# Performance work log

Measured on AMD Instinct MI355X. Metric: run time of the kernel, lower is better.

Reference implementation:

```python
import jax, jax.numpy as jnp
import numpy as np

B, T, C = 2, 2048, 1024
LAT = 256
N_HEAD = 16
HEAD_DIM = C // N_HEAD
SCALE = 1.0 / np.sqrt(HEAD_DIM).astype(np.float32)


def setup_inputs() -> dict:
    key = jax.random.key(0)
    ks = jax.random.split(key, 9)
    s_in = 0.02  # small init so softmax is well-conditioned
    return {
        "x": jax.random.normal(ks[0], (B, T, C), dtype=jnp.float32),
        "wq_lat": jax.random.normal(ks[1], (C, LAT), dtype=jnp.float32) * s_in,
        "wk_lat": jax.random.normal(ks[2], (C, LAT), dtype=jnp.float32) * s_in,
        "wv_lat": jax.random.normal(ks[3], (C, LAT), dtype=jnp.float32) * s_in,
        "wq_heads": jax.random.normal(ks[4], (LAT, C), dtype=jnp.float32) * s_in,
        "wk_heads": jax.random.normal(ks[5], (LAT, C), dtype=jnp.float32) * s_in,
        "wv_heads": jax.random.normal(ks[6], (LAT, C), dtype=jnp.float32) * s_in,
        "w_proj": jax.random.normal(ks[7], (C, C), dtype=jnp.float32) * s_in,
        "b_proj": jnp.zeros((C,), dtype=jnp.float32),
    }


def reference(x, wq_lat, wk_lat, wv_lat, wq_heads, wk_heads, wv_heads, w_proj, b_proj):
    Bx, Tx, Cx = x.shape
    # low-rank latent projections then up-projection to per-head q/k/v
    q = (x @ wq_lat) @ wq_heads  # [B,T,C]
    k = (x @ wk_lat) @ wk_heads
    v = (x @ wv_lat) @ wv_heads
    q = q.reshape(Bx, Tx, N_HEAD, HEAD_DIM).transpose(0, 2, 1, 3)  # [B,H,T,D]
    k = k.reshape(Bx, Tx, N_HEAD, HEAD_DIM).transpose(0, 2, 1, 3)
    v = v.reshape(Bx, Tx, N_HEAD, HEAD_DIM).transpose(0, 2, 1, 3)
    att = jnp.einsum("bhqd,bhkd->bhqk", q, k) * SCALE  # [B,H,T,T]
    causal = jnp.tril(jnp.ones((Tx, Tx), dtype=bool))
    att = jnp.where(causal[None, None], att, -jnp.inf)
    att = jax.nn.softmax(att, axis=-1)
    y = jnp.einsum("bhqk,bhkd->bhqd", att, v)  # [B,H,T,D]
    y = y.transpose(0, 2, 1, 3).reshape(Bx, Tx, Cx)
    return y @ w_proj + b_proj
```

## Files before the change

kernel.cpp:

```cpp
#include <hip/hip_runtime.h>

#define SCALE 0.125f
#define SL 0.18033688011112042f

typedef __bf16 bf16x8 __attribute__((ext_vector_type(8)));
typedef short short4v __attribute__((ext_vector_type(4)));
typedef unsigned short u16x4 __attribute__((ext_vector_type(4)));
typedef float f32x4 __attribute__((ext_vector_type(4)));
typedef unsigned int uint2v __attribute__((ext_vector_type(2)));

__device__ __forceinline__ unsigned short f2b(float f) {
  unsigned u = __float_as_uint(f);
  u += 0x7fffu + ((u >> 16) & 1u);
  return (unsigned short)(u >> 16);
}
__device__ __forceinline__ float ex2(float x) {
  float r;
  asm("v_exp_f32 %0, %1" : "=v"(r) : "v"(x));
  return r;
}

#define GLB(p) ((__attribute__((address_space(1))) void*)(void*)(p))
#define LDSP(p) ((__attribute__((address_space(3))) void*)(p))

__global__ __launch_bounds__(256) void prep(
    const float* __restrict__ x, const float* __restrict__ wq_lat,
    const float* __restrict__ wk_lat, const float* __restrict__ wv_lat,
    const float* __restrict__ wq_h, const float* __restrict__ wk_h,
    const float* __restrict__ wv_h, const float* __restrict__ w_proj,
    unsigned short* __restrict__ x_bf, unsigned short* __restrict__ wlatT,
    unsigned short* __restrict__ whT, unsigned short* __restrict__ wpT) {
  __shared__ float tile[32][33];
  const int blk = blockIdx.x, tid = threadIdx.x;
  if (blk < 1024) {
    int i = blk * 256 + tid;
#pragma unroll
    for (int j = 0; j < 4; j++) {
      float4 v = ((const float4*)x)[i + j * 262144];
      u16x4 p;
      p.x = f2b(v.x); p.y = f2b(v.y); p.z = f2b(v.z); p.w = f2b(v.w);
      ((u16x4*)x_bf)[i + j * 262144] = p;
    }
  } else if (blk < 1792) {
    int idx = blk - 1024;
    int z = idx >> 8, rem = idx & 255;
    const float* wsrc = z == 0 ? wq_lat : (z == 1 ? wk_lat : wv_lat);
    unsigned short* o = wlatT + z * 262144;
    int c0 = (rem & 7) * 32, r0 = (rem >> 3) * 32;
    int tx = tid & 31, ty = tid >> 5;
#pragma unroll
    for (int i = 0; i < 32; i += 8) tile[ty + i][tx] = wsrc[(r0 + ty + i) * 256 + c0 + tx];
    __syncthreads();
#pragma unroll
    for (int i = 0; i < 32; i += 8) o[(c0 + ty + i) * 1024 + r0 + tx] = f2b(tile[tx][ty + i]);
  } else if (blk < 2560) {
    int idx = blk - 1792;
    int z = idx >> 8, rem = idx & 255;
    const float* wsrc = z == 0 ? wq_h : (z == 1 ? wk_h : wv_h);
    unsigned short* o = whT + z * 262144;
    int c0 = (rem & 31) * 32, r0 = (rem >> 5) * 32;
    int tx = tid & 31, ty = tid >> 5;
#pragma unroll
    for (int i = 0; i < 32; i += 8) tile[ty + i][tx] = wsrc[(r0 + ty + i) * 1024 + c0 + tx];
    __syncthreads();
#pragma unroll
    for (int i = 0; i < 32; i += 8) o[(c0 + ty + i) * 256 + r0 + tx] = f2b(tile[tx][ty + i]);
  } else {
    int idx = blk - 2560;
    int c0 = (idx & 31) * 32, r0 = (idx >> 5) * 32;
    int tx = tid & 31, ty = tid >> 5;
#pragma unroll
    for (int i = 0; i < 32; i += 8) tile[ty + i][tx] = w_proj[(r0 + ty + i) * 1024 + c0 + tx];
    __syncthreads();
#pragma unroll
    for (int i = 0; i < 32; i += 8) wpT[(c0 + ty + i) * 1024 + r0 + tx] = f2b(tile[tx][ty + i]);
  }
}

template <int MODE>
__global__ __launch_bounds__(256) void gemm_bt(
    const unsigned short* __restrict__ A0, const unsigned short* __restrict__ A1,
    const unsigned short* __restrict__ A2,
    const unsigned short* __restrict__ B0, const unsigned short* __restrict__ B1,
    const unsigned short* __restrict__ B2,
    void* __restrict__ C0, void* __restrict__ C1, void* __restrict__ C2,
    const float* __restrict__ bias, int M, int N, int K) {
  const int z = blockIdx.z;
  const unsigned short* A = z == 0 ? A0 : (z == 1 ? A1 : A2);
  const unsigned short* BT = z == 0 ? B0 : (z == 1 ? B1 : B2);
  void* C = z == 0 ? C0 : (z == 1 ? C1 : C2);

  __shared__ unsigned short lA[128 * 32];
  __shared__ unsigned short lB[128 * 32];

  const int t = threadIdx.x;
  const int n0 = blockIdx.x * 128;
  const int m0 = blockIdx.y * 128;
  const int lane = t & 63;
  const int wid = t >> 6;
  const int wr = wid >> 1, wc = wid & 1;
  const int lo = lane & 15, g = lane >> 4;

  f32x4 acc[4][4];
#pragma unroll
  for (int i = 0; i < 4; i++)
#pragma unroll
    for (int j = 0; j < 4; j++) acc[i][j] = (f32x4){0.f, 0.f, 0.f, 0.f};

  const unsigned short* ga = A + (size_t)(m0 + (t >> 2)) * K + (t & 3) * 8;
  const unsigned short* gb = BT + (size_t)(n0 + (t >> 2)) * K + (t & 3) * 8;
  const size_t rowK64 = (size_t)64 * K;

  for (int k0 = 0; k0 < K; k0 += 32) {
    __syncthreads();
    __builtin_amdgcn_global_load_lds(GLB(ga + k0), LDSP((char*)lA + t * 16), 16, 0, 0);
    __builtin_amdgcn_global_load_lds(GLB(ga + rowK64 + k0), LDSP((char*)lA + 4096 + t * 16), 16, 0, 0);
    __builtin_amdgcn_global_load_lds(GLB(gb + k0), LDSP((char*)lB + t * 16), 16, 0, 0);
    __builtin_amdgcn_global_load_lds(GLB(gb + rowK64 + k0), LDSP((char*)lB + 4096 + t * 16), 16, 0, 0);
    __syncthreads();

    bf16x8 af[4], bfr[4];
#pragma unroll
    for (int i = 0; i < 4; i++) {
      af[i] = *(const bf16x8*)&lA[(wr * 64 + i * 16 + lo) * 32 + g * 8];
      bfr[i] = *(const bf16x8*)&lB[(wc * 64 + i * 16 + lo) * 32 + g * 8];
    }
#pragma unroll
    for (int i = 0; i < 4; i++)
#pragma unroll
      for (int j = 0; j < 4; j++)
        acc[i][j] = __builtin_amdgcn_mfma_f32_16x16x32_bf16(af[i], bfr[j], acc[i][j], 0, 0, 0);
  }

  if constexpr (MODE == 2) {
    float* Cf = (float*)C;
#pragma unroll
    for (int i = 0; i < 4; i++) {
      int row0 = m0 + wr * 64 + i * 16 + g * 4;
#pragma unroll
      for (int j = 0; j < 4; j++) {
        int col = n0 + wc * 64 + j * 16 + lo;
        float bv = bias[col];
#pragma unroll
        for (int r = 0; r < 4; r++) Cf[(size_t)(row0 + r) * N + col] = acc[i][j][r] + bv;
      }
    }
  } else {
    unsigned short* Cb = (unsigned short*)C;
#pragma unroll
    for (int i = 0; i < 4; i++) {
      int row0 = m0 + wr * 64 + i * 16 + g * 4;
#pragma unroll
      for (int j = 0; j < 4; j++) {
        int col = n0 + wc * 64 + j * 16 + lo;
#pragma unroll
        for (int r = 0; r < 4; r++) Cb[(size_t)(row0 + r) * N + col] = f2b(acc[i][j][r]);
      }
    }
  }
}

__global__ __launch_bounds__(512) void gemm_up8(const unsigned short* __restrict__ A,
                                                const unsigned short* __restrict__ BT,
                                                unsigned short* __restrict__ Qo,
                                                unsigned short* __restrict__ Ko,
                                                unsigned short* __restrict__ Vo) {
  __shared__ char smem[131072];

  const int t = threadIdx.x;
  const int lane = t & 63;
  const int wid = t >> 6;
  const int wr = wid >> 2, wc = wid & 3;
  const int lo = lane & 15, g = lane >> 4;
  const int lin = blockIdx.x;
  const int xcd = lin & 7;
  const int slot = lin >> 3;
  const int by = (xcd << 1) | (slot >= 12 ? 1 : 0);
  const int bx = slot >= 12 ? slot - 12 : slot;
  const int m0 = by * 256;
  const int z = bx >> 2;
  const int ncb = (bx & 3) * 256;
  const unsigned short* Az = A + (size_t)z * 1048576;
  const unsigned short* Bz = BT + (size_t)z * 262144;

  const int slog8 = (((t & 3) ^ ((t >> 2) & 3) ^ (((t >> 4) & 1) << 1)) << 3);
  const unsigned short *aS00, *aS01, *aS10, *aS11, *bS00, *bS01, *bS10, *bS11;
  {
    const int r = t >> 2;
    aS00 = Az + (size_t)(m0 + r) * 256 + slog8;
    aS01 = Az + (size_t)(m0 + r + 128) * 256 + slog8;
    aS10 = aS00 + 32;
    aS11 = aS01 + 32;
    bS00 = Bz + (size_t)(ncb + r) * 256 + slog8;
    bS01 = Bz + (size_t)(ncb + r + 128) * 256 + slog8;
    bS10 = bS00 + 32;
    bS11 = bS01 + 32;
  }
  char* dA0 = smem + t * 16;
  char* dA1 = smem + 16384 + t * 16;
  char* dB0 = smem + 32768 + t * 16;
  char* dB1 = smem + 49152 + t * 16;

  const int slotA = ((g ^ (lo & 3) ^ (((lo >> 2) & 1) << 1)) << 4);
  const char* aR = smem + (wr * 128 + lo) * 64 + slotA;
  const char* bR = smem + 32768 + (wc * 64 + lo) * 64 + slotA;

  f32x4 acc[8][4];
#pragma unroll
  for (int i = 0; i < 8; i++)
#pragma unroll
    for (int j = 0; j < 4; j++) acc[i][j] = (f32x4){0.f, 0.f, 0.f, 0.f};

#define STG(p0, p1, dst, D)                                                              \
  __builtin_amdgcn_global_load_lds(GLB(p0), LDSP(dst + (D)*65536), 16, 0, 0);            \
  __builtin_amdgcn_global_load_lds(GLB(p1), LDSP(dst + (D)*65536 + 8192), 16, 0, 0);     \
  p0 += 64; p1 += 64;

#define MF16(FRB, af, bf)                                                                \
  __builtin_amdgcn_s_setprio(1);                                                         \
  _Pragma("unroll") for (int i = 0; i < 4; i++)                                          \
  _Pragma("unroll") for (int j = 0; j < 4; j++)                                          \
      acc[(FRB) + i][j] = __builtin_amdgcn_mfma_f32_16x16x32_bf16(af[i], bf[j],          \
                                                                  acc[(FRB) + i][j], 0, 0, 0); \
  __builtin_amdgcn_s_setprio(0);

#define TILE(D, S)                                                                       \
  {                                                                                      \
    bf16x8 af[4], bf[4];                                                                 \
    _Pragma("unroll") for (int j = 0; j < 4; j++)                                        \
        bf[j] = *(const bf16x8*)(bR + (D)*65536 + j * 1024);                             \
    _Pragma("unroll") for (int i = 0; i < 4; i++)                                        \
        af[i] = *(const bf16x8*)(aR + (D)*65536 + i * 1024);                             \
    if (S) { STG(aS00, aS01, dA0, (D) ^ 1); }                                            \
    __builtin_amdgcn_s_barrier();                                                        \
    MF16(0, af, bf);                                                                     \
    __builtin_amdgcn_s_barrier();                                                        \
    _Pragma("unroll") for (int i = 0; i < 4; i++)                                        \
        af[i] = *(const bf16x8*)(aR + (D)*65536 + (4 + i) * 1024);                       \
    if (S) { STG(bS00, bS01, dB0, (D) ^ 1); }                                            \
    __builtin_amdgcn_s_barrier();                                                        \
    MF16(4, af, bf);                                                                     \
    if (S) { asm volatile("s_waitcnt vmcnt(4)" ::: "memory"); }                          \
    else   { asm volatile("s_waitcnt vmcnt(0)" ::: "memory"); }                          \
    __builtin_amdgcn_s_barrier();                                                        \
    _Pragma("unroll") for (int j = 0; j < 4; j++)                                        \
        bf[j] = *(const bf16x8*)(bR + (D)*65536 + 16384 + j * 1024);                     \
    _Pragma("unroll") for (int i = 0; i < 4; i++)                                        \
        af[i] = *(const bf16x8*)(aR + (D)*65536 + 16384 + i * 1024);                     \
    if (S) { STG(aS10, aS11, dA1, (D) ^ 1); }                                            \
    __builtin_amdgcn_s_barrier();                                                        \
    MF16(0, af, bf);                                                                     \
    __builtin_amdgcn_s_barrier();                                                        \
    _Pragma("unroll") for (int i = 0; i < 4; i++)                                        \
        af[i] = *(const bf16x8*)(aR + (D)*65536 + 16384 + (4 + i) * 1024);               \
    if (S) { STG(bS10, bS11, dB1, (D) ^ 1); }                                            \
    __builtin_amdgcn_s_barrier();                                                        \
    MF16(4, af, bf);                                                                     \
    if (S) { asm volatile("s_waitcnt vmcnt(4)" ::: "memory"); }                          \
    __builtin_amdgcn_s_barrier();                                                        \
  }

  { STG(aS00, aS01, dA0, 0); }
  { STG(bS00, bS01, dB0, 0); }
  { STG(aS10, aS11, dA1, 0); }
  { STG(bS10, bS11, dB1, 0); }
  asm volatile("s_waitcnt vmcnt(0)" ::: "memory");
  __builtin_amdgcn_s_barrier();

  TILE(0, 1);
  TILE(1, 1);
  TILE(0, 1);
  TILE(1, 0);

#undef TILE
#undef MF16
#undef STG

  if (z < 2) {
    unsigned short* Cb = z == 0 ? Qo : Ko;
    const float scl = z == 0 ? SL : 1.0f;
#pragma unroll
    for (int fr = 0; fr < 8; fr++) {
      int row0 = m0 + wr * 128 + fr * 16 + g * 4;
#pragma unroll
      for (int fc = 0; fc < 4; fc++) {
        int col = ncb + wc * 64 + fc * 16 + lo;
#pragma unroll
        for (int r = 0; r < 4; r++) Cb[(size_t)(row0 + r) * 1024 + col] = f2b(acc[fr][fc][r] * scl);
      }
    }
  } else {
#pragma unroll
    for (int fr = 0; fr < 8; fr++) {
      int row0 = m0 + wr * 128 + fr * 16 + g * 4;
      int bb = row0 >> 11, tloc = row0 & 2047;
#pragma unroll
      for (int fc = 0; fc < 4; fc++) {
        int col = ncb + wc * 64 + fc * 16 + lo;
        u16x4 pk;
#pragma unroll
        for (int r = 0; r < 4; r++) pk[r] = f2b(acc[fr][fc][r]);
        *(u16x4*)&Vo[((size_t)(bb * 1024) + col) * 2048 + tloc] = pk;
      }
    }
  }
}

__global__ __launch_bounds__(256) void attn_fwd(const unsigned short* __restrict__ Q,
                                                const unsigned short* __restrict__ K,
                                                const unsigned short* __restrict__ VT,
                                                unsigned short* __restrict__ Y) {
  __shared__ char smem[32768];

  const int tid = threadIdx.x;
  const int w = tid >> 6;
  const int lane = tid & 63;
  const int lo = lane & 15, g = lane >> 4;
  const int lo7 = lo & 7;
  const int bid = blockIdx.x;
  const int bh = bid & 31;
  const int code = bid >> 5;
  const int qq = code >> 3, kk = code & 7;
  const int chunk = qq == 0 ? 31 - kk : (qq == 1 ? 16 + kk : (qq == 2 ? 15 - kk : kk));
  const int b = bh >> 4, h = bh & 15;
  const int q0 = chunk * 64 + w * 16;

  const unsigned short* Qb = Q + (size_t)(b * 2048) * 1024 + h * 64;
  const unsigned short* Kb = K + (size_t)(b * 2048) * 1024 + h * 64;
  const unsigned short* Vb = VT + (size_t)((b * 16 + h) * 64) * 2048;

  bf16x8 qf0 = *(const bf16x8*)(Qb + (size_t)(q0 + lo) * 1024 + g * 8);
  bf16x8 qf1 = *(const bf16x8*)(Qb + (size_t)(q0 + lo) * 1024 + 32 + g * 8);

  const f32x4 z4 = (f32x4){0.f, 0.f, 0.f, 0.f};
  f32x4 acc[4];
#pragma unroll
  for (int dt = 0; dt < 4; dt++) acc[dt] = z4;
  float lrun = 0.f;
  const int nt = chunk + 1;

  const int koff = lo * 128 + ((g ^ lo7) << 4);
  char* kb0 = smem + koff;
  char* kb1 = smem + (koff ^ 64);
  const int voff = lo * 128 + ((g ^ ((lo7 & 1) << 1)) << 3) + ((lo7 >> 1) << 5);
  char* vq0 = smem + 16384 + voff;
  char* vq1 = smem + 16384 + (voff ^ 32);
  char* vq2 = smem + 16384 + (voff ^ 64);
  char* vq3 = smem + 16384 + (voff ^ 96);

  const int r0s = tid >> 3, c0s = (tid & 7) ^ (r0s & 7);
  const unsigned short* sk0 = Kb + (size_t)r0s * 1024 + c0s * 8;
  const unsigned short* sk1 = sk0 + (size_t)32 * 1024;
  const unsigned short* sv0 = Vb + (size_t)r0s * 2048 + c0s * 8;
  const unsigned short* sv1 = sv0 + (size_t)32 * 2048;
  char* dk0 = smem + tid * 16;
  char* dk1 = smem + 4096 + tid * 16;
  char* dv0 = smem + 16384 + tid * 16;
  char* dv1 = smem + 20480 + tid * 16;

#define STAGE(BUF)                                                                        \
  __builtin_amdgcn_global_load_lds(GLB(sk0), LDSP(dk0 + (BUF)*8192), 16, 0, 0);           \
  __builtin_amdgcn_global_load_lds(GLB(sk1), LDSP(dk1 + (BUF)*8192), 16, 0, 0);           \
  __builtin_amdgcn_global_load_lds(GLB(sv0), LDSP(dv0 + (BUF)*8192), 16, 0, 0);           \
  __builtin_amdgcn_global_load_lds(GLB(sv1), LDSP(dv1 + (BUF)*8192), 16, 0, 0);           \
  sk0 += 65536; sk1 += 65536; sv0 += 64; sv1 += 64;

#define COMPUTE(k0v, BUF, MASKED)                                                         \
  {                                                                                       \
    bf16x8 kfA[4], kfB[4];                                                                \
    _Pragma("unroll") for (int kvf = 0; kvf < 4; kvf++) {                                 \
      kfA[kvf] = *(const bf16x8*)(kb0 + (BUF)*8192 + kvf * 2048);                         \
      kfB[kvf] = *(const bf16x8*)(kb1 + (BUF)*8192 + kvf * 2048);                         \
    }                                                                                     \
    short4v vf[4][4];                                                                     \
    _Pragma("unroll") for (int kvf = 0; kvf < 4; kvf++) {                                 \
      const char* vp = kvf == 0 ? vq0 : (kvf == 1 ? vq1 : (kvf == 2 ? vq2 : vq3));        \
      _Pragma("unroll") for (int dt = 0; dt < 4; dt++)                                    \
          vf[dt][kvf] = *(const short4v*)(vp + (BUF)*8192 + dt * 2048);                   \
    }                                                                                     \
    f32x4 st[4];                                                                          \
    __builtin_amdgcn_s_setprio(1);                                                        \
    _Pragma("unroll") for (int kvf = 0; kvf < 4; kvf++) {                                 \
      st[kvf] = __builtin_amdgcn_mfma_f32_16x16x32_bf16(kfA[kvf], qf0, z4, 0, 0, 0);      \
      st[kvf] = __builtin_amdgcn_mfma_f32_16x16x32_bf16(kfB[kvf], qf1, st[kvf], 0, 0, 0); \
    }                                                                                     \
    __builtin_amdgcn_s_setprio(0);                                                        \
    if (MASKED) {                                                                         \
      const int qg = q0 + lo;                                                             \
      _Pragma("unroll") for (int kvf = 0; kvf < 4; kvf++)                                 \
      _Pragma("unroll") for (int r = 0; r < 4; r++) {                                     \
        int tk = (k0v) + kvf * 16 + g * 4 + r;                                            \
        if (tk > qg) st[kvf][r] = -3.0e38f;                                               \
      }                                                                                   \
    }                                                                                     \
    __builtin_amdgcn_s_setprio(1);                                                        \
    _Pragma("unroll") for (int kvf = 0; kvf < 4; kvf++) {                                 \
      float p0 = ex2(st[kvf][0]);                                                         \
      float p1 = ex2(st[kvf][1]);                                                         \
      float p2 = ex2(st[kvf][2]);                                                         \
      float p3 = ex2(st[kvf][3]);                                                         \
      lrun += (p0 + p1) + (p2 + p3);                                                      \
      uint2v pw;                                                                          \
      pw.x = __builtin_amdgcn_perm(__float_as_uint(p1), __float_as_uint(p0), 0x07060302u); \
      pw.y = __builtin_amdgcn_perm(__float_as_uint(p3), __float_as_uint(p2), 0x07060302u); \
      short4v pb = __builtin_bit_cast(short4v, pw);                                       \
      _Pragma("unroll") for (int dt = 0; dt < 4; dt++)                                    \
          acc[dt] = __builtin_amdgcn_mfma_f32_16x16x16bf16_1k(vf[dt][kvf], pb,            \
                                                              acc[dt], 0, 0, 0);          \
    }                                                                                     \
    __builtin_amdgcn_s_setprio(0);                                                        \
  }

  STAGE(0);
  __syncthreads();
  int t = 0;
  for (; t + 2 <= nt - 1; t += 2) {
    STAGE(1);
    COMPUTE(t * 64, 0, false);
    __syncthreads();
    STAGE(0);
    COMPUTE(t * 64 + 64, 1, false);
    __syncthreads();
  }
  if (t < nt - 1) {
    STAGE(1);
    COMPUTE(t * 64, 0, false);
    __syncthreads();
    COMPUTE(t * 64 + 64, 1, true);
  } else {
    COMPUTE(t * 64, 0, true);
  }

  {
    float l = lrun;
    l += __shfl_xor(l, 16);
    l += __shfl_xor(l, 32);
    float inv = 1.0f / l;
    unsigned short* yp = Y + (size_t)(b * 2048 + q0 + lo) * 1024 + h * 64;
#pragma unroll
    for (int dt = 0; dt < 4; dt++) {
      float y0 = acc[dt][0] * inv, y1 = acc[dt][1] * inv;
      float y2 = acc[dt][2] * inv, y3 = acc[dt][3] * inv;
      uint2v pw;
      pw.x = __builtin_amdgcn_perm(__float_as_uint(y1), __float_as_uint(y0), 0x07060302u);
      pw.y = __builtin_amdgcn_perm(__float_as_uint(y3), __float_as_uint(y2), 0x07060302u);
      *(uint2v*)&yp[dt * 16 + g * 4] = pw;
    }
  }
#undef STAGE
#undef COMPUTE
}

extern "C" void kernel_launch(void* const* d_in, const int* in_sizes, int n_in,
                              void* d_out, int out_size, void* d_ws, size_t ws_size,
                              hipStream_t stream) {
  const float* x = (const float*)d_in[0];
  const float* wq_lat = (const float*)d_in[1];
  const float* wk_lat = (const float*)d_in[2];
  const float* wv_lat = (const float*)d_in[3];
  const float* wq_h = (const float*)d_in[4];
  const float* wk_h = (const float*)d_in[5];
  const float* wv_h = (const float*)d_in[6];
  const float* w_proj = (const float*)d_in[7];
  const float* b_proj = (const float*)d_in[8];
  float* out = (float*)d_out;

  char* ws = (char*)d_ws;
  unsigned short* x_bf = (unsigned short*)(ws + 0);
  unsigned short* wlatT = (unsigned short*)(ws + 8388608);
  unsigned short* whT = (unsigned short*)(ws + 9961472);
  unsigned short* wpT = (unsigned short*)(ws + 11534336);
  unsigned short* lat = (unsigned short*)(ws + 13631488);
  unsigned short* q_bf = (unsigned short*)(ws + 19922944);
  unsigned short* k_bf = (unsigned short*)(ws + 28311552);
  unsigned short* vT = (unsigned short*)(ws + 36700160);
  unsigned short* y_bf = (unsigned short*)(ws + 45088768);

  prep<<<3584, 256, 0, stream>>>(x, wq_lat, wk_lat, wv_lat, wq_h, wk_h, wv_h, w_proj,
                                 x_bf, wlatT, whT, wpT);

  gemm_bt<0><<<dim3(2, 32, 3), 256, 0, stream>>>(
      x_bf, x_bf, x_bf, wlatT, wlatT + 262144, wlatT + 524288,
      lat, lat + 1048576, lat + 2097152, nullptr, 4096, 256, 1024);

  gemm_up8<<<192, 512, 0, stream>>>(lat, whT, q_bf, k_bf, vT);

  attn_fwd<<<1024, 256, 0, stream>>>(q_bf, k_bf, vT, y_bf);

  gemm_bt<2><<<dim3(8, 32, 1), 256, 0, stream>>>(
      y_bf, y_bf, y_bf, wpT, wpT, wpT, out, out, out, b_proj, 4096, 1024, 1024);
}
```

Measured before the change: 112.0 us.

## Split attention KV tiles across waves and reduce partial accumulators via LDS

Changes the attention kernel's work split. Each wave now processes all 64 queries of the chunk against its own 16-key slice of each KV tile, where before each wave took 16 queries against all 64 keys. Per-wave partial outputs and row sums are combined through a two-stage LDS tree reduction, and wave 0 writes the result. This cuts per-wave LDS fragment loads of K and V, but adds a cross-wave reduction epilogue, larger register accumulators (16 f32x4) and extra shared memory.

Result: slower. 118.8 us (+6.1%).

```diff
diff --git a/kernel.cpp b/kernel.cpp
--- a/kernel.cpp
+++ b/kernel.cpp
@@ -310,7 +310,7 @@
                                                 const unsigned short* __restrict__ K,
                                                 const unsigned short* __restrict__ VT,
                                                 unsigned short* __restrict__ Y) {
-  __shared__ char smem[32768];
+  __shared__ char smem[36864];
 
   const int tid = threadIdx.x;
   const int w = tid >> 6;
@@ -323,30 +323,33 @@
   const int qq = code >> 3, kk = code & 7;
   const int chunk = qq == 0 ? 31 - kk : (qq == 1 ? 16 + kk : (qq == 2 ? 15 - kk : kk));
   const int b = bh >> 4, h = bh & 15;
-  const int q0 = chunk * 64 + w * 16;
+  const int q0b = chunk * 64;
 
   const unsigned short* Qb = Q + (size_t)(b * 2048) * 1024 + h * 64;
   const unsigned short* Kb = K + (size_t)(b * 2048) * 1024 + h * 64;
   const unsigned short* Vb = VT + (size_t)((b * 16 + h) * 64) * 2048;
 
-  bf16x8 qf0 = *(const bf16x8*)(Qb + (size_t)(q0 + lo) * 1024 + g * 8);
-  bf16x8 qf1 = *(const bf16x8*)(Qb + (size_t)(q0 + lo) * 1024 + 32 + g * 8);
+  bf16x8 qf[4][2];
+#pragma unroll
+  for (int qfi = 0; qfi < 4; qfi++)
+#pragma unroll
+    for (int sp = 0; sp < 2; sp++)
+      qf[qfi][sp] = *(const bf16x8*)(Qb + (size_t)(q0b + qfi * 16 + lo) * 1024 + sp * 32 + g * 8);
 
   const f32x4 z4 = (f32x4){0.f, 0.f, 0.f, 0.f};
-  f32x4 acc[4];
-#pragma unroll
-  for (int dt = 0; dt < 4; dt++) acc[dt] = z4;
-  float lrun = 0.f;
+  f32x4 acc[4][4];
+#pragma unroll
+  for (int qfi = 0; qfi < 4; qfi++)
+#pragma unroll
+    for (int dt = 0; dt < 4; dt++) acc[qfi][dt] = z4;
+  f32x4 lrunv = z4;
   const int nt = chunk + 1;
 
   const int koff = lo * 128 + ((g ^ lo7) << 4);
-  char* kb0 = smem + koff;
-  char* kb1 = smem + (koff ^ 64);
+  char* kb0 = smem + w * 2048 + koff;
+  char* kb1 = smem + w * 2048 + (koff ^ 64);
   const int voff = lo * 128 + ((g ^ ((lo7 & 1) << 1)) << 3) + ((lo7 >> 1) << 5);
-  char* vq0 = smem + 16384 + voff;
-  char* vq1 = smem + 16384 + (voff ^ 32);
-  char* vq2 = smem + 16384 + (voff ^ 64);
-  char* vq3 = smem + 16384 + (voff ^ 96);
+  char* vpw = smem + 16384 + (voff ^ (w << 5));
 
   const int r0s = tid >> 3, c0s = (tid & 7) ^ (r0s & 7);
   const unsigned short* sk0 = Kb + (size_t)r0s * 1024 + c0s * 8;
@@ -367,48 +370,40 @@
 
 #define COMPUTE(k0v, BUF, MASKED)                                                         \
   {                                                                                       \
-    bf16x8 kfA[4], kfB[4];                                                                \
-    _Pragma("unroll") for (int kvf = 0; kvf < 4; kvf++) {                                 \
-      kfA[kvf] = *(const bf16x8*)(kb0 + (BUF)*8192 + kvf * 2048);                         \
-      kfB[kvf] = *(const bf16x8*)(kb1 + (BUF)*8192 + kvf * 2048);                         \
-    }                                                                                     \
-    short4v vf[4][4];                                                                     \
-    _Pragma("unroll") for (int kvf = 0; kvf < 4; kvf++) {                                 \
-      const char* vp = kvf == 0 ? vq0 : (kvf == 1 ? vq1 : (kvf == 2 ? vq2 : vq3));        \
-      _Pragma("unroll") for (int dt = 0; dt < 4; dt++)                                    \
-          vf[dt][kvf] = *(const short4v*)(vp + (BUF)*8192 + dt * 2048);                   \
-    }                                                                                     \
-    f32x4 st[4];                                                                          \
-    __builtin_amdgcn_s_setprio(1);                                                        \
-    _Pragma("unroll") for (int kvf = 0; kvf < 4; kvf++) {                                 \
-      st[kvf] = __builtin_amdgcn_mfma_f32_16x16x32_bf16(kfA[kvf], qf0, z4, 0, 0, 0);      \
-      st[kvf] = __builtin_amdgcn_mfma_f32_16x16x32_bf16(kfB[kvf], qf1, st[kvf], 0, 0, 0); \
-    }                                                                                     \
-    __builtin_amdgcn_s_setprio(0);                                                        \
-    if (MASKED) {                                                                         \
-      const int qg = q0 + lo;                                                             \
-      _Pragma("unroll") for (int kvf = 0; kvf < 4; kvf++)                                 \
-      _Pragma("unroll") for (int r = 0; r < 4; r++) {                                     \
-        int tk = (k0v) + kvf * 16 + g * 4 + r;                                            \
-        if (tk > qg) st[kvf][r] = -3.0e38f;                                               \
+    bf16x8 kfA = *(const bf16x8*)(kb0 + (BUF)*8192);                                      \
+    bf16x8 kfB = *(const bf16x8*)(kb1 + (BUF)*8192);                                      \
+    short4v vf0 = *(const short4v*)(vpw + (BUF)*8192);                                    \
+    short4v vf1 = *(const short4v*)(vpw + (BUF)*8192 + 2048);                             \
+    short4v vf2 = *(const short4v*)(vpw + (BUF)*8192 + 4096);                             \
+    short4v vf3 = *(const short4v*)(vpw + (BUF)*8192 + 6144);                             \
+    const int tkb = (k0v) + (w << 4) + g * 4;                                             \
+    _Pragma("unroll") for (int qfi = 0; qfi < 4; qfi++) {                                 \
+      f32x4 st;                                                                           \
+      __builtin_amdgcn_s_setprio(1);                                                      \
+      st = __builtin_amdgcn_mfma_f32_16x16x32_bf16(kfA, qf[qfi][0], z4, 0, 0, 0);         \
+      st = __builtin_amdgcn_mfma_f32_16x16x32_bf16(kfB, qf[qfi][1], st, 0, 0, 0);         \
+      __builtin_amdgcn_s_setprio(0);                                                      \
+      if (MASKED) {                                                                       \
+        const int qg = q0b + qfi * 16 + lo;                                               \
+        _Pragma("unroll") for (int r = 0; r < 4; r++)                                     \
+            if (tkb + r > qg) st[r] = -3.0e38f;                                           \
       }                                                                                   \
-    }                                                                                     \
-    __builtin_amdgcn_s_setprio(1);                                                        \
-    _Pragma("unroll") for (int kvf = 0; kvf < 4; kvf++) {                                 \
-      float p0 = ex2(st[kvf][0]);                                                         \
-      float p1 = ex2(st[kvf][1]);                                                         \
-      float p2 = ex2(st[kvf][2]);                                                         \
-      float p3 = ex2(st[kvf][3]);                                                         \
-      lrun += (p0 + p1) + (p2 + p3);                                                      \
+      float p0 = ex2(st[0]);                                                              \
+      float p1 = ex2(st[1]);                                                              \
+      float p2 = ex2(st[2]);                                                              \
+      float p3 = ex2(st[3]);                                                              \
+      lrunv[qfi] += (p0 + p1) + (p2 + p3);                                                \
       uint2v pw;                                                                          \
       pw.x = __builtin_amdgcn_perm(__float_as_uint(p1), __float_as_uint(p0), 0x07060302u); \
       pw.y = __builtin_amdgcn_perm(__float_as_uint(p3), __float_as_uint(p2), 0x07060302u); \
       short4v pb = __builtin_bit_cast(short4v, pw);                                       \
-      _Pragma("unroll") for (int dt = 0; dt < 4; dt++)                                    \
-          acc[dt] = __builtin_amdgcn_mfma_f32_16x16x16bf16_1k(vf[dt][kvf], pb,            \
-                                                              acc[dt], 0, 0, 0);          \
+      __builtin_amdgcn_s_setprio(1);                                                      \
+      acc[qfi][0] = __builtin_amdgcn_mfma_f32_16x16x16bf16_1k(vf0, pb, acc[qfi][0], 0, 0, 0); \
+      acc[qfi][1] = __builtin_amdgcn_mfma_f32_16x16x16bf16_1k(vf1, pb, acc[qfi][1], 0, 0, 0); \
+      acc[qfi][2] = __builtin_amdgcn_mfma_f32_16x16x16bf16_1k(vf2, pb, acc[qfi][2], 0, 0, 0); \
+      acc[qfi][3] = __builtin_amdgcn_mfma_f32_16x16x16bf16_1k(vf3, pb, acc[qfi][3], 0, 0, 0); \
+      __builtin_amdgcn_s_setprio(0);                                                      \
     }                                                                                     \
-    __builtin_amdgcn_s_setprio(0);                                                        \
   }
 
   STAGE(0);
@@ -431,20 +426,71 @@
     COMPUTE(t * 64, 0, true);
   }
 
-  {
-    float l = lrun;
-    l += __shfl_xor(l, 16);
-    l += __shfl_xor(l, 32);
-    float inv = 1.0f / l;
-    unsigned short* yp = Y + (size_t)(b * 2048 + q0 + lo) * 1024 + h * 64;
-#pragma unroll
-    for (int dt = 0; dt < 4; dt++) {
-      float y0 = acc[dt][0] * inv, y1 = acc[dt][1] * inv;
-      float y2 = acc[dt][2] * inv, y3 = acc[dt][3] * inv;
-      uint2v pw;
-      pw.x = __builtin_amdgcn_perm(__float_as_uint(y1), __float_as_uint(y0), 0x07060302u);
-      pw.y = __builtin_amdgcn_perm(__float_as_uint(y3), __float_as_uint(y2), 0x07060302u);
-      *(uint2v*)&yp[dt * 16 + g * 4] = pw;
+#pragma unroll
+  for (int qfi = 0; qfi < 4; qfi++) {
+    lrunv[qfi] += __shfl_xor(lrunv[qfi], 16);
+    lrunv[qfi] += __shfl_xor(lrunv[qfi], 32);
+  }
+  __syncthreads();
+  float* regA = (float*)smem;
+  float* regB = (float*)(smem + 16384);
+  float* lreg = (float*)(smem + 32768);
+
+  if (w == 1 || w == 3) {
+    float* dst = (w == 1) ? regA : regB;
+#pragma unroll
+    for (int qfi = 0; qfi < 4; qfi++)
+#pragma unroll
+      for (int dt = 0; dt < 4; dt++)
+        *(f32x4*)&dst[(qfi * 4 + dt) * 256 + lane * 4] = acc[qfi][dt];
+  }
+  *(f32x4*)&lreg[w * 256 + lane * 4] = lrunv;
+  __syncthreads();
+  if (w == 0) {
+#pragma unroll
+    for (int qfi = 0; qfi < 4; qfi++)
+#pragma unroll
+      for (int dt = 0; dt < 4; dt++)
+        acc[qfi][dt] += *(const f32x4*)&regA[(qfi * 4 + dt) * 256 + lane * 4];
+    lrunv += *(const f32x4*)&lreg[1 * 256 + lane * 4];
+  } else if (w == 2) {
+#pragma unroll
+    for (int qfi = 0; qfi < 4; qfi++)
+#pragma unroll
+      for (int dt = 0; dt < 4; dt++)
+        acc[qfi][dt] += *(const f32x4*)&regB[(qfi * 4 + dt) * 256 + lane * 4];
+    lrunv += *(const f32x4*)&lreg[3 * 256 + lane * 4];
+  }
+  __syncthreads();
+  if (w == 2) {
+#pragma unroll
+    for (int qfi = 0; qfi < 4; qfi++)
+#pragma unroll
+      for (int dt = 0; dt < 4; dt++)
+        *(f32x4*)&regA[(qfi * 4 + dt) * 256 + lane * 4] = acc[qfi][dt];
+    *(f32x4*)&lreg[2 * 256 + lane * 4] = lrunv;
+  }
+  __syncthreads();
+  if (w == 0) {
+#pragma unroll
+    for (int qfi = 0; qfi < 4; qfi++)
+#pragma unroll
+      for (int dt = 0; dt < 4; dt++)
+        acc[qfi][dt] += *(const f32x4*)&regA[(qfi * 4 + dt) * 256 + lane * 4];
+    lrunv += *(const f32x4*)&lreg[2 * 256 + lane * 4];
+#pragma unroll
+    for (int qfi = 0; qfi < 4; qfi++) {
+      float inv = 1.0f / lrunv[qfi];
+      unsigned short* yp = Y + (size_t)(b * 2048 + q0b + qfi * 16 + lo) * 1024 + h * 64;
+#pragma unroll
+      for (int dt = 0; dt < 4; dt++) {
+        float y0 = acc[qfi][dt][0] * inv, y1 = acc[qfi][dt][1] * inv;
+        float y2 = acc[qfi][dt][2] * inv, y3 = acc[qfi][dt][3] * inv;
+        uint2v pw;
+        pw.x = __builtin_amdgcn_perm(__float_as_uint(y1), __float_as_uint(y0), 0x07060302u);
+        pw.y = __builtin_amdgcn_perm(__float_as_uint(y3), __float_as_uint(y2), 0x07060302u);
+        *(uint2v*)&yp[dt * 16 + g * 4] = pw;
+      }
     }
   }
 #undef STAGE
```

## Double-buffer LDS tiles in GEMM to overlap global loads with MFMA

Applied to the files above, without the earlier changes.

Replaces the single-buffered GEMM main loop with a two-stage ping-pong LDS buffer. The next K-slice is prefetched with global_load_lds while MFMAs run on the current slice, and the two __syncthreads per iteration become one waitcnt plus barrier per stage. s_setprio is also raised around the MFMA block. LDS use doubles to 32KB per block, which may lower occupancy, and the loop assumes K is a multiple of 32.

After: 98.56 us. 1.14x faster.

```diff
diff --git a/kernel.cpp b/kernel.cpp
--- a/kernel.cpp
+++ b/kernel.cpp
@@ -90,8 +90,7 @@
   const unsigned short* BT = z == 0 ? B0 : (z == 1 ? B1 : B2);
   void* C = z == 0 ? C0 : (z == 1 ? C1 : C2);
 
-  __shared__ unsigned short lA[128 * 32];
-  __shared__ unsigned short lB[128 * 32];
+  __shared__ char smem[32768];
 
   const int t = threadIdx.x;
   const int n0 = blockIdx.x * 128;
@@ -110,27 +109,46 @@
   const unsigned short* ga = A + (size_t)(m0 + (t >> 2)) * K + (t & 3) * 8;
   const unsigned short* gb = BT + (size_t)(n0 + (t >> 2)) * K + (t & 3) * 8;
   const size_t rowK64 = (size_t)64 * K;
-
-  for (int k0 = 0; k0 < K; k0 += 32) {
-    __syncthreads();
-    __builtin_amdgcn_global_load_lds(GLB(ga + k0), LDSP((char*)lA + t * 16), 16, 0, 0);
-    __builtin_amdgcn_global_load_lds(GLB(ga + rowK64 + k0), LDSP((char*)lA + 4096 + t * 16), 16, 0, 0);
-    __builtin_amdgcn_global_load_lds(GLB(gb + k0), LDSP((char*)lB + t * 16), 16, 0, 0);
-    __builtin_amdgcn_global_load_lds(GLB(gb + rowK64 + k0), LDSP((char*)lB + 4096 + t * 16), 16, 0, 0);
-    __syncthreads();
-
-    bf16x8 af[4], bfr[4];
-#pragma unroll
-    for (int i = 0; i < 4; i++) {
-      af[i] = *(const bf16x8*)&lA[(wr * 64 + i * 16 + lo) * 32 + g * 8];
-      bfr[i] = *(const bf16x8*)&lB[(wc * 64 + i * 16 + lo) * 32 + g * 8];
-    }
-#pragma unroll
-    for (int i = 0; i < 4; i++)
-#pragma unroll
-      for (int j = 0; j < 4; j++)
-        acc[i][j] = __builtin_amdgcn_mfma_f32_16x16x32_bf16(af[i], bfr[j], acc[i][j], 0, 0, 0);
-  }
+  char* dA = smem + t * 16;
+  char* dB = smem + 16384 + t * 16;
+  const char* rA = smem + (wr * 64 + lo) * 64 + g * 16;
+  const char* rB = smem + 16384 + (wc * 64 + lo) * 64 + g * 16;
+
+#define STGB(D, kof)                                                                     \
+  __builtin_amdgcn_global_load_lds(GLB(ga + (kof)), LDSP(dA + (D)*8192), 16, 0, 0);      \
+  __builtin_amdgcn_global_load_lds(GLB(ga + rowK64 + (kof)), LDSP(dA + (D)*8192 + 4096), 16, 0, 0); \
+  __builtin_amdgcn_global_load_lds(GLB(gb + (kof)), LDSP(dB + (D)*8192), 16, 0, 0);      \
+  __builtin_amdgcn_global_load_lds(GLB(gb + rowK64 + (kof)), LDSP(dB + (D)*8192 + 4096), 16, 0, 0);
+
+#define COMPB(D)                                                                         \
+  {                                                                                      \
+    bf16x8 af[4], bfr[4];                                                                \
+    _Pragma("unroll") for (int i = 0; i < 4; i++) {                                      \
+      af[i] = *(const bf16x8*)(rA + (D)*8192 + i * 1024);                                \
+      bfr[i] = *(const bf16x8*)(rB + (D)*8192 + i * 1024);                               \
+    }                                                                                    \
+    __builtin_amdgcn_s_setprio(1);                                                       \
+    _Pragma("unroll") for (int i = 0; i < 4; i++)                                        \
+    _Pragma("unroll") for (int j = 0; j < 4; j++)                                        \
+        acc[i][j] = __builtin_amdgcn_mfma_f32_16x16x32_bf16(af[i], bfr[j], acc[i][j], 0, 0, 0); \
+    __builtin_amdgcn_s_setprio(0);                                                       \
+  }
+
+  STGB(0, 0);
+  asm volatile("s_waitcnt vmcnt(0)" ::: "memory");
+  __builtin_amdgcn_s_barrier();
+  for (int k0 = 0; k0 < K; k0 += 64) {
+    if (k0 + 32 < K) { STGB(1, k0 + 32); }
+    COMPB(0);
+    asm volatile("s_waitcnt vmcnt(0)" ::: "memory");
+    __builtin_amdgcn_s_barrier();
+    if (k0 + 64 < K) { STGB(0, k0 + 64); }
+    COMPB(1);
+    asm volatile("s_waitcnt vmcnt(0)" ::: "memory");
+    __builtin_amdgcn_s_barrier();
+  }
+#undef STGB
+#undef COMPB
 
   if constexpr (MODE == 2) {
     float* Cf = (float*)C;
```
